# Kernel optimization log

Measured on AMD Instinct MI355X. Metric: run time of the kernel, lower is better.

Reference implementation:

```python
import jax, jax.numpy as jnp
import numpy as np

N_QUBITS = 13
DEPTH = 4
DIM = 2 ** N_QUBITS
PI = 3.141592653589793

# qubit 0 = most significant bit of the basis-state index
_idx = np.arange(DIM)
BITS = np.stack([(_idx >> (N_QUBITS - 1 - q)) & 1 for q in range(N_QUBITS)], axis=1)  # (DIM, n)
SIGNS = jnp.asarray(1.0 - 2.0 * BITS, dtype=jnp.float32)                               # Z eigenvalues, (DIM, n)
PARITY = jnp.asarray((-1.0) ** BITS.sum(axis=1), dtype=jnp.float32)                    # <Z^{(x)n}> diagonal, (DIM,)
# CZ entangling chain (q, q+1): diagonal (-1)^{sum_q b_q b_{q+1}}
ENT = jnp.asarray((-1.0) ** (BITS[:, :-1] * BITS[:, 1:]).sum(axis=1), dtype=jnp.float32)


def fwht(psi):
    """Normalized fast Walsh-Hadamard transform (H on every qubit), psi: (B, DIM) complex."""
    B = psi.shape[0]
    for q in range(N_QUBITS):
        psi = psi.reshape(B, 2 ** q, 2, -1)
        psi = jnp.stack([psi[:, :, 0] + psi[:, :, 1], psi[:, :, 0] - psi[:, :, 1]], axis=2)
    return psi.reshape(B, DIM) * (2.0 ** (-N_QUBITS / 2))


def feature_map_state(x):
    """Havlicek ZZ feature map: psi = D(x) H^n D(x) H^n |0...0>.
    Diagonal phase per basis state b: sum_j x_j s_j(b) + sum_{j<k} (pi-x_j)(pi-x_k) s_j(b) s_k(b)."""
    a = PI - x                                              # (B, n)
    u = x @ SIGNS.T                                         # (B, DIM)
    v = a @ SIGNS.T                                         # (B, DIM)
    phi = u + 0.5 * (v * v - jnp.sum(a * a, axis=1, keepdims=True))  # pair term via (sum)^2 trick
    d = jnp.exp(1j * phi)                                   # complex64 diagonal
    psi = jnp.full((x.shape[0], DIM), DIM ** -0.5, dtype=jnp.complex64)  # H^n |0>
    psi = fwht(d * psi)
    return d * psi


def _apply_1q(psi, U, q):
    """Apply 2x2 complex gate U to qubit q (bit-sliced)."""
    B = psi.shape[0]
    psi = psi.reshape(B, 2 ** q, 2, -1)
    a0, a1 = psi[:, :, 0], psi[:, :, 1]
    out = jnp.stack([U[0, 0] * a0 + U[0, 1] * a1, U[1, 0] * a0 + U[1, 1] * a1], axis=2)
    return out.reshape(B, DIM)


def variational_apply(psi, theta):
    """(DEPTH+1) layers of per-qubit Rz(b)Ry(a), CZ-chain entanglers between layers."""
    th = theta.reshape(DEPTH + 1, N_QUBITS, 2)
    for l in range(DEPTH + 1):
        if l > 0:
            psi = psi * ENT
        for q in range(N_QUBITS):
            ca = jnp.cos(0.5 * th[l, q, 0])
            sa = jnp.sin(0.5 * th[l, q, 0])
            em = jnp.exp(-0.5j * th[l, q, 1])
            ep = jnp.exp(0.5j * th[l, q, 1])
            U = jnp.stack([jnp.stack([em * ca, -em * sa]), jnp.stack([ep * sa, ep * ca])])
            psi = _apply_1q(psi, U, q)
    return psi


def setup_inputs() -> dict:
    key = jax.random.key(0)
    k1, k2 = jax.random.split(key)
    x = jax.random.normal(k1, (512, N_QUBITS), dtype=jnp.float32)
    theta = 0.1 * jax.random.normal(k2, ((DEPTH + 1) * N_QUBITS * 2,), dtype=jnp.float32)
    bias = jnp.zeros((1,), dtype=jnp.float32)
    return {"x": x, "theta": theta, "bias": bias}


def reference(x, theta, bias):
    psi = feature_map_state(x)
    psi = variational_apply(psi, theta)
    prob = psi.real ** 2 + psi.imag ** 2              # (B, DIM)
    logit = prob @ PARITY + bias[0]                   # (B,)
    return jnp.stack([-logit, logit], axis=1)         # two-class logits
```

## Files before the change

### kernel.cpp

```cpp
#include <hip/hip_runtime.h>
#include <hip/hip_bf16.h>

#define NQ   13
#define DIM  8192
#define PI_F 3.14159265358979323846f
#define NT   256
#define NAMP 32

__device__ __forceinline__ int lslot(int i) { return i + (i >> 5); }
#define NSLOT (DIM + (DIM >> 5))

__device__ __forceinline__ void rsincos(float x, float* s, float* c) {
  const float INV2PI = 0.15915494309189535f;
  const float TWOPI  = 6.283185307179586f;
  float r = x * INV2PI;
  r -= rintf(r);
  float ang = r * TWOPI;
  *s = __sinf(ang);
  *c = __cosf(ang);
}

template<int PAT>
__device__ __forceinline__ int ampIndex(int t, int j) {
  if constexpr (PAT == 0) return (t << 5) | j;
  else if constexpr (PAT == 1) return ((t >> 5) << 10) | (j << 5) | (t & 31);
  else return ((j >> 2) << 10) | (t << 2) | (j & 3);
}

template<int PAT>
__device__ __forceinline__ void buildTree(const float* __restrict__ w, float bias,
                                          int t, float* s) {
  float base = bias;
  if constexpr (PAT == 0) {
    #pragma unroll
    for (int k = 0; k < 8; k++) base += ((t >> k) & 1) ? w[5 + k] : 0.0f;
  } else if constexpr (PAT == 1) {
    #pragma unroll
    for (int k = 0; k < 5; k++) base += ((t >> k) & 1) ? w[k] : 0.0f;
    #pragma unroll
    for (int k = 0; k < 3; k++) base += ((t >> (5 + k)) & 1) ? w[10 + k] : 0.0f;
  } else {
    #pragma unroll
    for (int k = 0; k < 8; k++) base += ((t >> k) & 1) ? w[2 + k] : 0.0f;
  }
  constexpr int P[5] = { (PAT == 1) ? 5 : 0,
                         (PAT == 1) ? 6 : 1,
                         (PAT == 0) ? 2 : ((PAT == 1) ? 7 : 10),
                         (PAT == 0) ? 3 : ((PAT == 1) ? 8 : 11),
                         (PAT == 0) ? 4 : ((PAT == 1) ? 9 : 12) };
  s[0] = base;
  #pragma unroll
  for (int k = 0; k < 5; k++) {
    float wp = w[P[k]];
    #pragma unroll
    for (int m = 0; m < (1 << k); m++) s[m | (1 << k)] = s[m] + wp;
  }
}

template<int PAT>
__device__ __forceinline__ void loadAmps(const float* __restrict__ sRe,
                                         const float* __restrict__ sIm,
                                         int t, float* re, float* im) {
  #pragma unroll
  for (int j = 0; j < NAMP; j++) {
    int a = lslot(ampIndex<PAT>(t, j));
    re[j] = sRe[a]; im[j] = sIm[a];
  }
}

template<int PAT>
__device__ __forceinline__ void storeAmps(float* __restrict__ sRe,
                                          float* __restrict__ sIm,
                                          int t, const float* re, const float* im) {
  #pragma unroll
  for (int j = 0; j < NAMP; j++) {
    int a = lslot(ampIndex<PAT>(t, j));
    sRe[a] = re[j]; sIm[a] = im[j];
  }
}

template<int KB>
__device__ __forceinline__ void fwht_bit(float* re, float* im) {
  #pragma unroll
  for (int j = 0; j < NAMP; j++) if (!(j & (1 << KB))) {
    int j1 = j | (1 << KB);
    float r0 = re[j], i0 = im[j], r1 = re[j1], i1 = im[j1];
    re[j]  = r0 + r1; im[j]  = i0 + i1;
    re[j1] = r0 - r1; im[j1] = i0 - i1;
  }
}
__device__ __forceinline__ void fwht_all5(float* re, float* im) {
  fwht_bit<0>(re, im); fwht_bit<1>(re, im); fwht_bit<2>(re, im);
  fwht_bit<3>(re, im); fwht_bit<4>(re, im);
}

template<int KB>
__device__ __forceinline__ void applyRy(float* re, float* im, float ca, float sa) {
  #pragma unroll
  for (int j = 0; j < NAMP; j++) if (!(j & (1 << KB))) {
    int j1 = j | (1 << KB);
    float r0 = re[j], i0 = im[j], r1 = re[j1], i1 = im[j1];
    re[j]  = ca * r0 - sa * r1;  im[j]  = ca * i0 - sa * i1;
    re[j1] = sa * r0 + ca * r1;  im[j1] = sa * i0 + ca * i1;
  }
}

template<int PAT>
__device__ __forceinline__ void applyDiag(float* re, float* im,
                                          const float* __restrict__ wb,
                                          float bias, int t) {
  float rho[NAMP];
  buildTree<PAT>(wb, bias, t, rho);
  #pragma unroll
  for (int j = 0; j < NAMP; j++) {
    int i = ampIndex<PAT>(t, j);
    float sn, cs;
    rsincos(rho[j], &sn, &cs);
    float ent = (__popc(i & (i >> 1)) & 1) ? -1.0f : 1.0f;
    cs *= ent; sn *= ent;
    float r = re[j], q = im[j];
    re[j] = r * cs - q * sn;
    im[j] = r * sn + q * cs;
  }
}

__global__ __launch_bounds__(NT, 2) void qc_kernel(
    const float* __restrict__ xin,
    const float* __restrict__ thin,
    const float* __restrict__ bin,
    float* __restrict__ out) {
  __shared__ float sRe[NSLOT];
  __shared__ float sIm[NSLOT];
  __shared__ float gCA[65], gSA[65];
  __shared__ float gBbit[65];
  __shared__ float wX[13], wA[13];
  __shared__ float cons[8];
  __shared__ float red[NT / 64];

  const int t = threadIdx.x;
  const int b = blockIdx.x;

  if (t < NQ) {
    float xq = xin[b * NQ + t];
    float aq = PI_F - xq;
    wX[12 - t] = -2.0f * xq;
    wA[12 - t] = -2.0f * aq;
  }
  if (t < 65) {
    float av = thin[2 * t];
    float bv = thin[2 * t + 1];
    gCA[t] = cosf(0.5f * av);
    gSA[t] = sinf(0.5f * av);
    int l = t / NQ, q = t % NQ;
    gBbit[l * NQ + (12 - q)] = bv;
  }
  __syncthreads();
  if (t == 0) {
    float X = 0.f, A = 0.f, A2 = 0.f;
    for (int p = 0; p < NQ; p++) {
      float xq = -0.5f * wX[p], aq = -0.5f * wA[p];
      X += xq; A += aq; A2 += aq * aq;
    }
    cons[0] = X; cons[1] = A; cons[2] = A2;
    for (int l = 0; l < 5; l++) {
      float s = 0.f;
      for (int p = 0; p < NQ; p++) s += gBbit[l * NQ + p];
      cons[3 + l] = -0.5f * s;
    }
  }
  __syncthreads();

  float re[NAMP], im[NAMP];

  {
    float u[NAMP], v[NAMP];
    buildTree<0>(wX, cons[0], t, u);
    buildTree<0>(wA, cons[1], t, v);
    float A2 = cons[2];
    #pragma unroll
    for (int j = 0; j < NAMP; j++) {
      float phi = u[j] + 0.5f * (v[j] * v[j] - A2);
      float sn, cs; rsincos(phi, &sn, &cs);
      re[j] = cs; im[j] = sn;
    }
    fwht_all5(re, im);
    storeAmps<0>(sRe, sIm, t, re, im);
  }
  __syncthreads();

  loadAmps<1>(sRe, sIm, t, re, im);
  fwht_all5(re, im);
  storeAmps<1>(sRe, sIm, t, re, im);
  __syncthreads();

  loadAmps<2>(sRe, sIm, t, re, im);
  fwht_bit<2>(re, im); fwht_bit<3>(re, im); fwht_bit<4>(re, im);
  {
    float u[NAMP], v[NAMP];
    buildTree<2>(wX, cons[0], t, u);
    buildTree<2>(wA, cons[1], t, v);
    float A2 = cons[2];
    #pragma unroll
    for (int j = 0; j < NAMP; j++) {
      float phi = u[j] + 0.5f * (v[j] * v[j] - A2);
      float sn, cs; rsincos(phi, &sn, &cs);
      float r = re[j], q = im[j];
      re[j] = r * cs - q * sn;
      im[j] = r * sn + q * cs;
    }
  }
  storeAmps<2>(sRe, sIm, t, re, im);
  __syncthreads();

  float acc = 0.0f;
  for (int l = 0; l < 5; l++) {
    const int g = l * NQ;
    loadAmps<0>(sRe, sIm, t, re, im);
    if (l > 0) applyDiag<0>(re, im, gBbit + (l - 1) * NQ, cons[3 + (l - 1)], t);
    applyRy<0>(re, im, gCA[g + 12], gSA[g + 12]);
    applyRy<1>(re, im, gCA[g + 11], gSA[g + 11]);
    applyRy<2>(re, im, gCA[g + 10], gSA[g + 10]);
    applyRy<3>(re, im, gCA[g + 9],  gSA[g + 9]);
    applyRy<4>(re, im, gCA[g + 8],  gSA[g + 8]);
    storeAmps<0>(sRe, sIm, t, re, im);
    __syncthreads();
    loadAmps<1>(sRe, sIm, t, re, im);
    applyRy<0>(re, im, gCA[g + 7], gSA[g + 7]);
    applyRy<1>(re, im, gCA[g + 6], gSA[g + 6]);
    applyRy<2>(re, im, gCA[g + 5], gSA[g + 5]);
    applyRy<3>(re, im, gCA[g + 4], gSA[g + 4]);
    applyRy<4>(re, im, gCA[g + 3], gSA[g + 3]);
    storeAmps<1>(sRe, sIm, t, re, im);
    __syncthreads();
    loadAmps<2>(sRe, sIm, t, re, im);
    applyRy<2>(re, im, gCA[g + 2], gSA[g + 2]);
    applyRy<3>(re, im, gCA[g + 1], gSA[g + 1]);
    applyRy<4>(re, im, gCA[g + 0], gSA[g + 0]);
    if (l < 4) {
      storeAmps<2>(sRe, sIm, t, re, im);
      __syncthreads();
    } else {
      #pragma unroll
      for (int j = 0; j < NAMP; j++) {
        int i = ampIndex<2>(t, j);
        float p = re[j] * re[j] + im[j] * im[j];
        acc += (__popc(i) & 1) ? -p : p;
      }
    }
  }

  #pragma unroll
  for (int off = 32; off > 0; off >>= 1) acc += __shfl_down(acc, off, 64);
  if ((t & 63) == 0) red[t >> 6] = acc;
  __syncthreads();
  if (t == 0) {
    float total = red[0] + red[1] + red[2] + red[3];
    float logit = total * (1.0f / 67108864.0f) + bin[0];
    out[b * 2 + 0] = -logit;
    out[b * 2 + 1] = logit;
  }
}

extern "C" void kernel_launch(void* const* d_in, const int* in_sizes, int n_in,
                              void* d_out, int out_size, void* d_ws, size_t ws_size,
                              hipStream_t stream) {
  const float* x  = (const float*)d_in[0];
  const float* th = (const float*)d_in[1];
  const float* bi = (const float*)d_in[2];
  float* out = (float*)d_out;
  int B = in_sizes[0] / NQ;
  qc_kernel<<<B, NT, 0, stream>>>(x, th, bi, out);
}
```

Measured before the change: 110.0 us.

## Use 512 threads with 16 amplitudes each and regroup qubit passes across layers

Halves per-thread amplitudes (16 instead of 32) and doubles threads per block, so register pressure drops and more waves are resident. The qubit groupings are re-planned into seven bit patterns so that the layer boundary (last Ry, CZ diagonal, first Ry of the next layer) shares a single shared-memory pass. The diagonal phase is now built from precomputed complex exponentials by multiplication instead of one sincos per amplitude. In exchange there are more shared-memory passes per layer (4-qubit groups instead of 5) and more barriers.

```diff
diff --git a/kernel.cpp b/kernel.cpp
--- a/kernel.cpp
+++ b/kernel.cpp
@@ -1,11 +1,10 @@
 #include <hip/hip_runtime.h>
-#include <hip/hip_bf16.h>
 
 #define NQ   13
 #define DIM  8192
+#define NT   512
+#define NAMP 16
 #define PI_F 3.14159265358979323846f
-#define NT   256
-#define NAMP 32
 
 __device__ __forceinline__ int lslot(int i) { return i + (i >> 5); }
 #define NSLOT (DIM + (DIM >> 5))
@@ -20,62 +19,62 @@
   *c = __cosf(ang);
 }
 
-template<int PAT>
-__device__ __forceinline__ int ampIndex(int t, int j) {
-  if constexpr (PAT == 0) return (t << 5) | j;
-  else if constexpr (PAT == 1) return ((t >> 5) << 10) | (j << 5) | (t & 31);
-  else return ((j >> 2) << 10) | (t << 2) | (j & 3);
-}
-
-template<int PAT>
+template<int P> struct Pat;
+template<> struct Pat<0> { static constexpr int W[4] = {0,1,2,3};
+  static constexpr int N[9] = {4,5,6,7,8,9,10,11,12};
+  static __device__ __forceinline__ int idx(int t, int j) { return (t << 4) | j; } };
+template<> struct Pat<1> { static constexpr int W[4] = {4,5,6,7};
+  static constexpr int N[9] = {0,1,2,3,8,9,10,11,12};
+  static __device__ __forceinline__ int idx(int t, int j) { return ((t >> 4) << 8) | (j << 4) | (t & 15); } };
+template<> struct Pat<2> { static constexpr int W[4] = {8,9,10,11};
+  static constexpr int N[9] = {0,1,2,3,4,5,6,7,12};
+  static __device__ __forceinline__ int idx(int t, int j) { return ((t >> 8) << 12) | (j << 8) | (t & 255); } };
+template<> struct Pat<3> { static constexpr int W[4] = {0,1,2,12};
+  static constexpr int N[9] = {3,4,5,6,7,8,9,10,11};
+  static __device__ __forceinline__ int idx(int t, int j) { return ((j & 8) << 9) | (t << 3) | (j & 7); } };
+template<> struct Pat<4> { static constexpr int W[4] = {3,4,5,6};
+  static constexpr int N[9] = {0,1,2,7,8,9,10,11,12};
+  static __device__ __forceinline__ int idx(int t, int j) { return ((t >> 3) << 7) | (j << 3) | (t & 7); } };
+template<> struct Pat<5> { static constexpr int W[4] = {7,8,9,10};
+  static constexpr int N[9] = {0,1,2,3,4,5,6,11,12};
+  static __device__ __forceinline__ int idx(int t, int j) { return ((t >> 7) << 11) | (j << 7) | (t & 127); } };
+template<> struct Pat<6> { static constexpr int W[4] = {0,1,2,11};
+  static constexpr int N[9] = {3,4,5,6,7,8,9,10,12};
+  static __device__ __forceinline__ int idx(int t, int j) { return ((t & 256) << 4) | ((j & 8) << 8) | ((t & 255) << 3) | (j & 7); } };
+
+template<int P>
+__device__ __forceinline__ void loadAmps(const float* __restrict__ sRe,
+                                         const float* __restrict__ sIm,
+                                         int t, float* re, float* im) {
+  #pragma unroll
+  for (int j = 0; j < NAMP; j++) {
+    int a = lslot(Pat<P>::idx(t, j));
+    re[j] = sRe[a]; im[j] = sIm[a];
+  }
+}
+template<int P>
+__device__ __forceinline__ void storeAmps(float* __restrict__ sRe,
+                                          float* __restrict__ sIm,
+                                          int t, const float* re, const float* im) {
+  #pragma unroll
+  for (int j = 0; j < NAMP; j++) {
+    int a = lslot(Pat<P>::idx(t, j));
+    sRe[a] = re[j]; sIm[a] = im[j];
+  }
+}
+
+template<int P>
 __device__ __forceinline__ void buildTree(const float* __restrict__ w, float bias,
                                           int t, float* s) {
   float base = bias;
-  if constexpr (PAT == 0) {
-    #pragma unroll
-    for (int k = 0; k < 8; k++) base += ((t >> k) & 1) ? w[5 + k] : 0.0f;
-  } else if constexpr (PAT == 1) {
-    #pragma unroll
-    for (int k = 0; k < 5; k++) base += ((t >> k) & 1) ? w[k] : 0.0f;
-    #pragma unroll
-    for (int k = 0; k < 3; k++) base += ((t >> (5 + k)) & 1) ? w[10 + k] : 0.0f;
-  } else {
-    #pragma unroll
-    for (int k = 0; k < 8; k++) base += ((t >> k) & 1) ? w[2 + k] : 0.0f;
-  }
-  constexpr int P[5] = { (PAT == 1) ? 5 : 0,
-                         (PAT == 1) ? 6 : 1,
-                         (PAT == 0) ? 2 : ((PAT == 1) ? 7 : 10),
-                         (PAT == 0) ? 3 : ((PAT == 1) ? 8 : 11),
-                         (PAT == 0) ? 4 : ((PAT == 1) ? 9 : 12) };
+  #pragma unroll
+  for (int k = 0; k < 9; k++) base += ((t >> k) & 1) ? w[Pat<P>::N[k]] : 0.0f;
   s[0] = base;
   #pragma unroll
-  for (int k = 0; k < 5; k++) {
-    float wp = w[P[k]];
+  for (int k = 0; k < 4; k++) {
+    float wp = w[Pat<P>::W[k]];
     #pragma unroll
     for (int m = 0; m < (1 << k); m++) s[m | (1 << k)] = s[m] + wp;
-  }
-}
-
-template<int PAT>
-__device__ __forceinline__ void loadAmps(const float* __restrict__ sRe,
-                                         const float* __restrict__ sIm,
-                                         int t, float* re, float* im) {
-  #pragma unroll
-  for (int j = 0; j < NAMP; j++) {
-    int a = lslot(ampIndex<PAT>(t, j));
-    re[j] = sRe[a]; im[j] = sIm[a];
-  }
-}
-
-template<int PAT>
-__device__ __forceinline__ void storeAmps(float* __restrict__ sRe,
-                                          float* __restrict__ sIm,
-                                          int t, const float* re, const float* im) {
-  #pragma unroll
-  for (int j = 0; j < NAMP; j++) {
-    int a = lslot(ampIndex<PAT>(t, j));
-    sRe[a] = re[j]; sIm[a] = im[j];
   }
 }
 
@@ -89,9 +88,8 @@
     re[j1] = r0 - r1; im[j1] = i0 - i1;
   }
 }
-__device__ __forceinline__ void fwht_all5(float* re, float* im) {
-  fwht_bit<0>(re, im); fwht_bit<1>(re, im); fwht_bit<2>(re, im);
-  fwht_bit<3>(re, im); fwht_bit<4>(re, im);
+__device__ __forceinline__ void fwht_all4(float* re, float* im) {
+  fwht_bit<0>(re, im); fwht_bit<1>(re, im); fwht_bit<2>(re, im); fwht_bit<3>(re, im);
 }
 
 template<int KB>
@@ -105,26 +103,79 @@
   }
 }
 
-template<int PAT>
+template<int P, int KB>
+__device__ __forceinline__ void ryOn(float* re, float* im,
+                                     const float* __restrict__ gCA,
+                                     const float* __restrict__ gSA, int l) {
+  constexpr int q = 12 - Pat<P>::W[KB];
+  int g = l * NQ + q;
+  applyRy<KB>(re, im, gCA[g], gSA[g]);
+}
+template<int P>
+__device__ __forceinline__ void ry4(float* re, float* im,
+                                    const float* __restrict__ gCA,
+                                    const float* __restrict__ gSA, int l) {
+  ryOn<P, 0>(re, im, gCA, gSA, l);
+  ryOn<P, 1>(re, im, gCA, gSA, l);
+  ryOn<P, 2>(re, im, gCA, gSA, l);
+  ryOn<P, 3>(re, im, gCA, gSA, l);
+}
+
+template<int P, bool INIT>
+__device__ __forceinline__ void featureDiag(float* re, float* im,
+                                            const float* __restrict__ wX,
+                                            const float* __restrict__ wA,
+                                            const float* __restrict__ cons, int t) {
+  float u[NAMP], v[NAMP];
+  buildTree<P>(wX, cons[0], t, u);
+  buildTree<P>(wA, cons[1], t, v);
+  float A2 = cons[2];
+  #pragma unroll
+  for (int j = 0; j < NAMP; j++) {
+    float phi = u[j] + 0.5f * (v[j] * v[j] - A2);
+    float sn, cs; rsincos(phi, &sn, &cs);
+    if constexpr (INIT) { re[j] = cs; im[j] = sn; }
+    else {
+      float r = re[j], q = im[j];
+      re[j] = r * cs - q * sn;
+      im[j] = r * sn + q * cs;
+    }
+  }
+}
+
+template<int P>
 __device__ __forceinline__ void applyDiag(float* re, float* im,
                                           const float* __restrict__ wb,
+                                          const float* __restrict__ eR,
+                                          const float* __restrict__ eI,
                                           float bias, int t) {
-  float rho[NAMP];
-  buildTree<PAT>(wb, bias, t, rho);
+  float base = bias;
+  #pragma unroll
+  for (int k = 0; k < 9; k++) base += ((t >> k) & 1) ? wb[Pat<P>::N[k]] : 0.0f;
+  float cR[NAMP], cI[NAMP];
+  rsincos(base, &cI[0], &cR[0]);
+  #pragma unroll
+  for (int k = 0; k < 4; k++) {
+    float er = eR[Pat<P>::W[k]], ei = eI[Pat<P>::W[k]];
+    #pragma unroll
+    for (int m = 0; m < (1 << k); m++) {
+      float r0 = cR[m], i0 = cI[m];
+      cR[m | (1 << k)] = r0 * er - i0 * ei;
+      cI[m | (1 << k)] = r0 * ei + i0 * er;
+    }
+  }
   #pragma unroll
   for (int j = 0; j < NAMP; j++) {
-    int i = ampIndex<PAT>(t, j);
-    float sn, cs;
-    rsincos(rho[j], &sn, &cs);
-    float ent = (__popc(i & (i >> 1)) & 1) ? -1.0f : 1.0f;
-    cs *= ent; sn *= ent;
+    int i = Pat<P>::idx(t, j);
+    float sgn = (__popc(i & (i >> 1)) & 1) ? -1.0f : 1.0f;
+    float cs = cR[j] * sgn, sn = cI[j] * sgn;
     float r = re[j], q = im[j];
     re[j] = r * cs - q * sn;
     im[j] = r * sn + q * cs;
   }
 }
 
-__global__ __launch_bounds__(NT, 2) void qc_kernel(
+__global__ __launch_bounds__(NT, 4) void qc_kernel(
     const float* __restrict__ xin,
     const float* __restrict__ thin,
     const float* __restrict__ bin,
@@ -133,6 +184,7 @@
   __shared__ float sIm[NSLOT];
   __shared__ float gCA[65], gSA[65];
   __shared__ float gBbit[65];
+  __shared__ float eBr[65], eBi[65];
   __shared__ float wX[13], wA[13];
   __shared__ float cons[8];
   __shared__ float red[NT / 64];
@@ -152,7 +204,10 @@
     gCA[t] = cosf(0.5f * av);
     gSA[t] = sinf(0.5f * av);
     int l = t / NQ, q = t % NQ;
-    gBbit[l * NQ + (12 - q)] = bv;
+    int s = l * NQ + (12 - q);
+    gBbit[s] = bv;
+    eBr[s] = cosf(bv);
+    eBi[s] = sinf(bv);
   }
   __syncthreads();
   if (t == 0) {
@@ -172,80 +227,62 @@
 
   float re[NAMP], im[NAMP];
 
-  {
-    float u[NAMP], v[NAMP];
-    buildTree<0>(wX, cons[0], t, u);
-    buildTree<0>(wA, cons[1], t, v);
-    float A2 = cons[2];
-    #pragma unroll
-    for (int j = 0; j < NAMP; j++) {
-      float phi = u[j] + 0.5f * (v[j] * v[j] - A2);
-      float sn, cs; rsincos(phi, &sn, &cs);
-      re[j] = cs; im[j] = sn;
-    }
-    fwht_all5(re, im);
-    storeAmps<0>(sRe, sIm, t, re, im);
-  }
+  featureDiag<0, true>(re, im, wX, wA, cons, t);
+  fwht_all4(re, im);
+  storeAmps<0>(sRe, sIm, t, re, im);
   __syncthreads();
 
   loadAmps<1>(sRe, sIm, t, re, im);
-  fwht_all5(re, im);
+  fwht_all4(re, im);
   storeAmps<1>(sRe, sIm, t, re, im);
   __syncthreads();
 
   loadAmps<2>(sRe, sIm, t, re, im);
-  fwht_bit<2>(re, im); fwht_bit<3>(re, im); fwht_bit<4>(re, im);
-  {
-    float u[NAMP], v[NAMP];
-    buildTree<2>(wX, cons[0], t, u);
-    buildTree<2>(wA, cons[1], t, v);
-    float A2 = cons[2];
-    #pragma unroll
-    for (int j = 0; j < NAMP; j++) {
-      float phi = u[j] + 0.5f * (v[j] * v[j] - A2);
-      float sn, cs; rsincos(phi, &sn, &cs);
-      float r = re[j], q = im[j];
-      re[j] = r * cs - q * sn;
-      im[j] = r * sn + q * cs;
-    }
-  }
+  fwht_all4(re, im);
   storeAmps<2>(sRe, sIm, t, re, im);
   __syncthreads();
 
+  loadAmps<3>(sRe, sIm, t, re, im);
+  fwht_bit<3>(re, im);
+  featureDiag<3, false>(re, im, wX, wA, cons, t);
+  ry4<3>(re, im, gCA, gSA, 0);
+  storeAmps<3>(sRe, sIm, t, re, im);
+  __syncthreads();
+
   float acc = 0.0f;
+  #pragma unroll 1
   for (int l = 0; l < 5; l++) {
-    const int g = l * NQ;
-    loadAmps<0>(sRe, sIm, t, re, im);
-    if (l > 0) applyDiag<0>(re, im, gBbit + (l - 1) * NQ, cons[3 + (l - 1)], t);
-    applyRy<0>(re, im, gCA[g + 12], gSA[g + 12]);
-    applyRy<1>(re, im, gCA[g + 11], gSA[g + 11]);
-    applyRy<2>(re, im, gCA[g + 10], gSA[g + 10]);
-    applyRy<3>(re, im, gCA[g + 9],  gSA[g + 9]);
-    applyRy<4>(re, im, gCA[g + 8],  gSA[g + 8]);
-    storeAmps<0>(sRe, sIm, t, re, im);
+    loadAmps<4>(sRe, sIm, t, re, im);
+    ry4<4>(re, im, gCA, gSA, l);
+    storeAmps<4>(sRe, sIm, t, re, im);
     __syncthreads();
-    loadAmps<1>(sRe, sIm, t, re, im);
-    applyRy<0>(re, im, gCA[g + 7], gSA[g + 7]);
-    applyRy<1>(re, im, gCA[g + 6], gSA[g + 6]);
-    applyRy<2>(re, im, gCA[g + 5], gSA[g + 5]);
-    applyRy<3>(re, im, gCA[g + 4], gSA[g + 4]);
-    applyRy<4>(re, im, gCA[g + 3], gSA[g + 3]);
-    storeAmps<1>(sRe, sIm, t, re, im);
+    loadAmps<5>(sRe, sIm, t, re, im);
+    ry4<5>(re, im, gCA, gSA, l);
+    storeAmps<5>(sRe, sIm, t, re, im);
     __syncthreads();
-    loadAmps<2>(sRe, sIm, t, re, im);
-    applyRy<2>(re, im, gCA[g + 2], gSA[g + 2]);
-    applyRy<3>(re, im, gCA[g + 1], gSA[g + 1]);
-    applyRy<4>(re, im, gCA[g + 0], gSA[g + 0]);
-    if (l < 4) {
-      storeAmps<2>(sRe, sIm, t, re, im);
+    if (l == 4) {
+      loadAmps<6>(sRe, sIm, t, re, im);
+      ryOn<6, 3>(re, im, gCA, gSA, 4);
+      #pragma unroll
+      for (int j = 0; j < NAMP; j++) {
+        int i = Pat<6>::idx(t, j);
+        float p2 = re[j] * re[j] + im[j] * im[j];
+        acc += (__popc(i) & 1) ? -p2 : p2;
+      }
+    } else if ((l & 1) == 0) {
+      loadAmps<6>(sRe, sIm, t, re, im);
+      ryOn<6, 3>(re, im, gCA, gSA, l);
+      applyDiag<6>(re, im, gBbit + l * NQ, eBr + l * NQ, eBi + l * NQ, cons[3 + l], t);
+      ry4<6>(re, im, gCA, gSA, l + 1);
+      storeAmps<6>(sRe, sIm, t, re, im);
       __syncthreads();
     } else {
-      #pragma unroll
-      for (int j = 0; j < NAMP; j++) {
-        int i = ampIndex<2>(t, j);
-        float p = re[j] * re[j] + im[j] * im[j];
-        acc += (__popc(i) & 1) ? -p : p;
-      }
+      loadAmps<3>(sRe, sIm, t, re, im);
+      ryOn<3, 3>(re, im, gCA, gSA, l);
+      applyDiag<3>(re, im, gBbit + l * NQ, eBr + l * NQ, eBi + l * NQ, cons[3 + l], t);
+      ry4<3>(re, im, gCA, gSA, l + 1);
+      storeAmps<3>(sRe, sIm, t, re, im);
+      __syncthreads();
     }
   }
 
@@ -254,7 +291,9 @@
   if ((t & 63) == 0) red[t >> 6] = acc;
   __syncthreads();
   if (t == 0) {
-    float total = red[0] + red[1] + red[2] + red[3];
+    float total = 0.f;
+    #pragma unroll
+    for (int w = 0; w < NT / 64; w++) total += red[w];
     float logit = total * (1.0f / 67108864.0f) + bin[0];
     out[b * 2 + 0] = -logit;
     out[b * 2 + 1] = logit;
```

After: 135.0 us. 22.7% more time.
